# Performance work log

Measured on AMD Instinct MI355X. Metric: run time of the kernel, lower is better.

Reference implementation:

```python
import jax, jax.numpy as jnp
import numpy as np

N, IN, H, OUT, E = 4096, 128, 128, 2, 131072


def _hgnn(x, G, W, b):
    # HGNNConv (Feng et al.): X' = G @ (X W + b), G dense normalized [N,N]
    return G @ (x @ W + b)


def _mha(xin, Wqkv, bqkv, Wo, bo, nh):
    # torch.nn.MultiheadAttention, input (L, B, E), self-attention, eval mode
    L, B, Emb = xin.shape
    hd = Emb // nh
    qkv = xin @ Wqkv.T + bqkv                       # [L,B,3E]
    q, k, v = jnp.split(qkv, 3, axis=-1)
    def sh(t):
        return t.reshape(L, B, nh, hd).transpose(1, 2, 0, 3)  # [B,nh,L,hd]
    q, k, v = sh(q), sh(k), sh(v)
    att = jax.nn.softmax(jnp.einsum('bnld,bnmd->bnlm', q, k) / jnp.sqrt(jnp.float32(hd)), axis=-1)
    o = jnp.einsum('bnlm,bnmd->bnld', att, v).transpose(2, 0, 1, 3).reshape(L, B, Emb)
    return o @ Wo.T + bo


def setup_inputs() -> dict:
    key = jax.random.key(0)
    ks = jax.random.split(key, 40)
    d = {}
    d['x'] = jax.random.normal(ks[0], (N, IN), jnp.float32)
    # dense normalized hypergraph propagation matrices (rand, scaled ~1/N so rows sum ~1)
    d['hg_1hop'] = jax.random.uniform(ks[1], (N, N), jnp.float32) * (2.0 / N)
    d['hg_3hop'] = jax.random.uniform(ks[2], (N, N), jnp.float32) * (2.0 / N)
    d['edge_indices'] = jax.random.randint(ks[3], (2, E), 0, N).astype(jnp.int32)
    d['new_idb'] = jax.random.permutation(ks[4], N).astype(jnp.int32)
    d['lam'] = jax.random.uniform(ks[5], (1,), jnp.float32)
    d['beta'] = jnp.asarray(0.3, jnp.float32)
    i = 6
    def w(shape, s):
        nonlocal i
        out = jax.random.normal(ks[i], shape, jnp.float32) * s
        i += 1
        return out
    sw = 1.0 / np.sqrt(H)
    d['W1'] = w((IN, H), 1.0 / np.sqrt(IN)); d['b1'] = w((H,), 0.01)
    for nm in ['W2', 'W3', 'W1h', 'W3h', 'W2m', 'W3m']:
        d[nm] = w((H, H), sw); d['b' + nm[1:]] = w((H,), 0.01)
    for tag in ['mix', 'fus']:
        d['Wqkv_' + tag] = w((3 * H, H), sw); d['bqkv_' + tag] = w((3 * H,), 0.01)
        d['Wo_' + tag] = w((H, H), sw); d['bo_' + tag] = w((H,), 0.01)
    d['Wc'] = w((2 * H, OUT), 1.0 / np.sqrt(2 * H)); d['bc'] = w((OUT,), 0.01)
    return d


def reference(x, hg_1hop, hg_3hop, edge_indices, new_idb, lam, beta,
              W1, b1, W2, b2, W3, b3, W1h, b1h, W3h, b3h, W2m, b2m, W3m, b3m,
              Wqkv_mix, bqkv_mix, Wo_mix, bo_mix,
              Wqkv_fus, bqkv_fus, Wo_fus, bo_fus, Wc, bc):
    # eval mode: dropout = identity
    h1 = jax.nn.relu(_hgnn(x, hg_1hop, W1, b1))
    h2 = jax.nn.relu(_hgnn(h1, hg_1hop, W2, b2) + h1)
    h3_c1 = jax.nn.relu(_hgnn(h2, hg_1hop, W3, b3) + h2)

    # shuffle_hypergraph: permute nodes of the dense incidence-derived matrix
    hg1_b = hg_1hop[new_idb][:, new_idb]
    hg3_b = hg_3hop[new_idb][:, new_idb]
    l = lam[0]
    # mixup_hidden: manifold mixup of propagated features with permuted graph/features
    h1_mix_1hop = l * _hgnn(h1, hg_1hop, W1h, b1h) + (1.0 - l) * _hgnn(h1[new_idb], hg1_b, W1h, b1h)
    h1_mix_3hop = l * _hgnn(h1, hg_3hop, W3h, b3h) + (1.0 - l) * _hgnn(h1[new_idb], hg3_b, W3h, b3h)

    h1_stack = jnp.stack([h1_mix_1hop, h1_mix_3hop], axis=0)     # [2,N,H]
    h1_mix = _mha(h1_stack, Wqkv_mix, bqkv_mix, Wo_mix, bo_mix, 2).mean(axis=0)
    h2_mix = jax.nn.relu(_hgnn(h1_mix, hg_1hop, W2m, b2m) + h1_mix)
    h3_c2 = jax.nn.relu(_hgnn(h2_mix, hg_1hop, W3m, b3m) + h2_mix) * beta

    h3_stack = jnp.stack([h3_c1, h3_c2], axis=0)                 # [2,N,H]
    h3 = _mha(h3_stack, Wqkv_fus, bqkv_fus, Wo_fus, bo_fus, 4).mean(axis=0)

    edge_emb = jnp.concatenate([h3[edge_indices[0]], h3[edge_indices[1]]], axis=1)  # [E,2H]
    edge_pred = edge_emb @ Wc + bc
    return edge_pred, h3
```

## Files before the change

kernel.cpp:

```cpp
#include <hip/hip_runtime.h>
#include <math.h>

typedef unsigned short u16;
typedef short s8v __attribute__((ext_vector_type(8)));
typedef float f4v __attribute__((ext_vector_type(4)));

__device__ inline float b2f(u16 u) {
    union { unsigned int i; float f; } v; v.i = ((unsigned int)u) << 16; return v.f;
}
__device__ inline u16 f2b(float f) {
    unsigned int x = __float_as_uint(f);
    return (u16)((x + 0x7fffu + ((x >> 16) & 1u)) >> 16);
}
__device__ inline float ldf(const void* p, size_t i, int f32) {
    return f32 ? ((const float*)p)[i] : b2f(((const u16*)p)[i]);
}
__device__ inline s8v load8(const void* p, size_t idx, int f32) {
    if (f32) {
        const float* f = (const float*)p + idx;
        float4 a = *(const float4*)(f);
        float4 b = *(const float4*)(f + 4);
        s8v r;
        r[0] = (short)f2b(a.x); r[1] = (short)f2b(a.y);
        r[2] = (short)f2b(a.z); r[3] = (short)f2b(a.w);
        r[4] = (short)f2b(b.x); r[5] = (short)f2b(b.y);
        r[6] = (short)f2b(b.z); r[7] = (short)f2b(b.w);
        return r;
    }
    return *(const s8v*)((const u16*)p + idx);
}

__global__ void detect_kernel(const u16* __restrict__ hg, int* __restrict__ flag) {
    int lane = threadIdx.x;
    bool ok = true;
    for (int i = 0; i < 32; ++i) {
        float v = b2f(hg[lane * 32 + i]);
        ok = ok && (fabsf(v) <= 1e-3f);
    }
    unsigned long long m = __ballot(ok);
    if (lane == 0) *flag = (m == ~0ull) ? 0 : 1;
}

__global__ __launch_bounds__(512) void big_gemm(const void* __restrict__ G,
                                                const u16* __restrict__ Zt,
                                                float* __restrict__ part,
                                                int kChunkLen,
                                                const int* __restrict__ dflag) {
    __shared__ u16 At[128 * 72];
    __shared__ u16 Bt[128 * 72];
    const int f32 = *dflag;
    const int tid = threadIdx.x;
    const int rowBase = blockIdx.x * 128;
    const int kChunk = blockIdx.y * kChunkLen;
    const int w = tid >> 6, lane = tid & 63;
    const int wm = w & 1, wn = w >> 1;
    const int l15 = lane & 15, quad = lane >> 4;
    const int nIter = kChunkLen >> 6;

    const int r0 = tid >> 3, kb0 = tid & 7;
    const int r1 = 64 + (tid >> 3), kb1 = tid & 7;

    f4v acc[4][2] = {};

    for (int it = 0; it < nIter; ++it) {
        const int kBase = kChunk + it * 64;
        s8v ga0 = load8(G, (size_t)(rowBase + r0) * 4096 + kBase + kb0 * 8, f32);
        s8v gb0 = *(const s8v*)(Zt + (size_t)r0 * 4096 + kBase + kb0 * 8);
        s8v ga1 = load8(G, (size_t)(rowBase + r1) * 4096 + kBase + kb1 * 8, f32);
        s8v gb1 = *(const s8v*)(Zt + (size_t)r1 * 4096 + kBase + kb1 * 8);
        __syncthreads();
        *(s8v*)(At + r0 * 72 + kb0 * 8) = ga0;
        *(s8v*)(Bt + r0 * 72 + kb0 * 8) = gb0;
        *(s8v*)(At + r1 * 72 + kb1 * 8) = ga1;
        *(s8v*)(Bt + r1 * 72 + kb1 * 8) = gb1;
        __syncthreads();
#pragma unroll
        for (int ks = 0; ks < 2; ++ks) {
            s8v a[4], b[2];
            const int kq = ks * 4 + quad;
#pragma unroll
            for (int mi = 0; mi < 4; ++mi)
                a[mi] = *(const s8v*)(At + (wm * 64 + mi * 16 + l15) * 72 + kq * 8);
#pragma unroll
            for (int ni = 0; ni < 2; ++ni)
                b[ni] = *(const s8v*)(Bt + (wn * 32 + ni * 16 + l15) * 72 + kq * 8);
#pragma unroll
            for (int mi = 0; mi < 4; ++mi)
#pragma unroll
                for (int ni = 0; ni < 2; ++ni)
                    acc[mi][ni] = __builtin_amdgcn_mfma_f32_16x16x32_bf16(
                        a[mi], b[ni], acc[mi][ni], 0, 0, 0);
        }
    }
    float* pbase = part + (size_t)blockIdx.y * 4096 * 128;
#pragma unroll
    for (int mi = 0; mi < 4; ++mi)
#pragma unroll
        for (int ni = 0; ni < 2; ++ni) {
            int row = rowBase + wm * 64 + mi * 16 + quad * 4;
            int col = wn * 32 + ni * 16 + l15;
#pragma unroll
            for (int r = 0; r < 4; ++r)
                pbase[(size_t)(row + r) * 128 + col] = acc[mi][ni][r];
        }
}

__global__ __launch_bounds__(256) void reduce_epi(const float* __restrict__ part,
                                                  const u16* __restrict__ res,
                                                  const void* __restrict__ betap,
                                                  u16* __restrict__ out, int mode,
                                                  int S, const int* __restrict__ dflag) {
    int i = (blockIdx.x * 256 + threadIdx.x) * 4;
    f4v t = {};
    for (int s = 0; s < S; ++s)
        t += *(const f4v*)(part + (size_t)s * 524288 + i);
    float bscale = (mode == 2) ? ldf(betap, 0, *dflag) : 1.0f;
    u16 o[4];
#pragma unroll
    for (int j = 0; j < 4; ++j) {
        float v = t[j];
        if (mode == 1 || mode == 2) v += b2f(res[i + j]);
        if (mode <= 2) v = fmaxf(v, 0.0f);
        if (mode == 2) v *= bscale;
        o[j] = f2b(v);
    }
    *(ushort4*)(out + i) = make_ushort4(o[0], o[1], o[2], o[3]);
}

__global__ __launch_bounds__(256) void feat_gemm(const void* __restrict__ A,
                                                 const void* __restrict__ W,
                                                 const void* __restrict__ bias,
                                                 void* __restrict__ out,
                                                 u16* __restrict__ mirror,
                                                 size_t outOfs,
                                                 int M, int NcTotal, int wLayout,
                                                 int outMode, int aRaw, int outRaw,
                                                 const int* __restrict__ dflag) {
    __shared__ char smem[52224];
    u16* Wt = (u16*)smem;
    u16* At = (u16*)(smem + 34816);
    u16* Tt = (u16*)smem;
    const int f32 = *dflag;
    const int aF32 = aRaw & f32;
    const int tid = threadIdx.x;
    const int rowBase = blockIdx.x * 64;
    const int colBase = blockIdx.y * 128;

    if (wLayout == 1) {
#pragma unroll
        for (int i = 0; i < 8; ++i) {
            int c = i * 256 + tid;
            int n = c >> 4, kb = c & 15;
            s8v v = load8(W, (size_t)(colBase + n) * 128 + kb * 8, f32);
            *(s8v*)(Wt + n * 136 + kb * 8) = v;
        }
    } else {
#pragma unroll
        for (int i = 0; i < 64; ++i) {
            int idx = i * 256 + tid;
            int k = idx >> 7, n = idx & 127;
            Wt[n * 136 + k] = f2b(ldf(W, (size_t)k * NcTotal + colBase + n, f32));
        }
    }
#pragma unroll
    for (int i = 0; i < 4; ++i) {
        int c = i * 256 + tid;
        int r = c >> 4, kb = c & 15;
        s8v v = load8(A, (size_t)(rowBase + r) * 128 + kb * 8, aF32);
        *(s8v*)(At + r * 136 + kb * 8) = v;
    }
    __syncthreads();

    const int w = tid >> 6, lane = tid & 63, l15 = lane & 15, quad = lane >> 4;
    f4v acc[8] = {};
#pragma unroll
    for (int ks = 0; ks < 4; ++ks) {
        int k = ks * 32 + quad * 8;
        s8v a = *(const s8v*)(At + (w * 16 + l15) * 136 + k);
#pragma unroll
        for (int ni = 0; ni < 8; ++ni) {
            s8v b = *(const s8v*)(Wt + (ni * 16 + l15) * 136 + k);
            acc[ni] = __builtin_amdgcn_mfma_f32_16x16x32_bf16(a, b, acc[ni], 0, 0, 0);
        }
    }

    if (outMode == 0) {
#pragma unroll
        for (int ni = 0; ni < 8; ++ni) {
            int n = colBase + ni * 16 + l15;
            float bv = ldf(bias, n, f32);
#pragma unroll
            for (int r = 0; r < 4; ++r) {
                int row = rowBase + w * 16 + quad * 4 + r;
                size_t idx = (size_t)row * NcTotal + n;
                float v = acc[ni][r] + bv;
                u16 vb = f2b(v);
                if (outRaw && f32) ((float*)out)[outOfs + idx] = v;
                else               ((u16*)out)[outOfs + idx] = vb;
                if (mirror) mirror[idx] = vb;
            }
        }
    } else {
        __syncthreads();
#pragma unroll
        for (int ni = 0; ni < 8; ++ni) {
            int n = ni * 16 + l15;
            float bv = ldf(bias, colBase + n, f32);
#pragma unroll
            for (int r = 0; r < 4; ++r)
                Tt[n * 72 + (w * 16 + quad * 4 + r)] = f2b(acc[ni][r] + bv);
        }
        __syncthreads();
#pragma unroll
        for (int i = 0; i < 4; ++i) {
            int c = i * 256 + tid;
            int h = c >> 3, nb = c & 7;
            s8v v = *(const s8v*)(Tt + h * 72 + nb * 8);
            *(s8v*)((u16*)out + (size_t)(colBase + h) * M + rowBase + nb * 8) = v;
        }
    }
}

__global__ __launch_bounds__(256) void mix_kernel(const u16* __restrict__ Ph1,
                                                  const u16* __restrict__ Ph3,
                                                  const int* __restrict__ perm,
                                                  const void* __restrict__ lamp,
                                                  u16* __restrict__ xin,
                                                  const int* __restrict__ dflag) {
    int i = blockIdx.x * 256 + threadIdx.x;
    int n = i >> 7, h = i & 127;
    float l = ldf(lamp, 0, *dflag);
    int pn = perm[n];
    float a = l * b2f(Ph1[i]) + (1.0f - l) * b2f(Ph1[(size_t)pn * 128 + h]);
    float b = l * b2f(Ph3[i]) + (1.0f - l) * b2f(Ph3[(size_t)pn * 128 + h]);
    xin[i] = f2b(a);
    xin[524288 + i] = f2b(b);
}

__global__ __launch_bounds__(256) void attn_kernel(const u16* __restrict__ qkv,
                                                   u16* __restrict__ obar, int nh) {
    int wid = threadIdx.x >> 6, lane = threadIdx.x & 63;
    int n = blockIdx.x * 4 + wid;
    const u16* r0 = qkv + (size_t)n * 384;
    const u16* r1 = qkv + (size_t)(4096 + n) * 384;
    int hd = 128 / nh;
    float scale = 1.0f / sqrtf((float)hd);
    float ov[2];
#pragma unroll
    for (int e = 0; e < 2; ++e) {
        int h = e * 64 + lane;
        float q0 = b2f(r0[h]),       q1 = b2f(r1[h]);
        float k0 = b2f(r0[128 + h]), k1 = b2f(r1[128 + h]);
        float v0 = b2f(r0[256 + h]), v1 = b2f(r1[256 + h]);
        float s00 = q0 * k0, s01 = q0 * k1, s10 = q1 * k0, s11 = q1 * k1;
        for (int off = hd >> 1; off; off >>= 1) {
            s00 += __shfl_xor(s00, off);
            s01 += __shfl_xor(s01, off);
            s10 += __shfl_xor(s10, off);
            s11 += __shfl_xor(s11, off);
        }
        s00 *= scale; s01 *= scale; s10 *= scale; s11 *= scale;
        float m0 = fmaxf(s00, s01), m1 = fmaxf(s10, s11);
        float e00 = expf(s00 - m0), e01 = expf(s01 - m0);
        float e10 = expf(s10 - m1), e11 = expf(s11 - m1);
        float a00 = e00 / (e00 + e01), a01 = e01 / (e00 + e01);
        float a10 = e10 / (e10 + e11), a11 = e11 / (e10 + e11);
        float o0 = a00 * v0 + a01 * v1;
        float o1 = a10 * v0 + a11 * v1;
        ov[e] = 0.5f * (o0 + o1);
    }
    obar[(size_t)n * 128 + lane] = f2b(ov[0]);
    obar[(size_t)n * 128 + 64 + lane] = f2b(ov[1]);
}

__global__ __launch_bounds__(256) void edge_kernel(const u16* __restrict__ h3,
                                                   const int* __restrict__ eidx,
                                                   const void* __restrict__ Wc,
                                                   const void* __restrict__ bc,
                                                   void* __restrict__ out,
                                                   const int* __restrict__ dflag) {
    __shared__ float w0[256], w1[256];
    const int f32 = *dflag;
    int t = threadIdx.x;
    w0[t] = ldf(Wc, (size_t)t * 2, f32);
    w1[t] = ldf(Wc, (size_t)t * 2 + 1, f32);
    __syncthreads();
    int e = blockIdx.x * 256 + t;
    float a0 = ldf(bc, 0, f32), a1 = ldf(bc, 1, f32);
#pragma unroll
    for (int p = 0; p < 2; ++p) {
        int node = eidx[p * 131072 + e];
        const s8v* row = (const s8v*)(h3 + (size_t)node * 128);
#pragma unroll
        for (int cch = 0; cch < 16; ++cch) {
            s8v d = row[cch];
#pragma unroll
            for (int j = 0; j < 8; ++j) {
                float f = b2f((u16)d[j]);
                int k = p * 128 + cch * 8 + j;
                a0 += f * w0[k];
                a1 += f * w1[k];
            }
        }
    }
    if (f32) {
        ((float*)out)[(size_t)e * 2] = a0;
        ((float*)out)[(size_t)e * 2 + 1] = a1;
    } else {
        ((u16*)out)[(size_t)e * 2] = f2b(a0);
        ((u16*)out)[(size_t)e * 2 + 1] = f2b(a1);
    }
}

extern "C" void kernel_launch(void* const* d_in, const int* in_sizes, int n_in,
                              void* d_out, int out_size, void* d_ws, size_t ws_size,
                              hipStream_t stream) {
    const void* x    = d_in[0];
    const void* G1   = d_in[1];
    const void* G3   = d_in[2];
    const int* eidx = (const int*)d_in[3];
    const int* perm = (const int*)d_in[4];
    const void* lam  = d_in[5];
    const void* beta = d_in[6];
    const void* W1 = d_in[7],  *b1 = d_in[8];
    const void* W2 = d_in[9],  *b2 = d_in[10];
    const void* W3 = d_in[11], *b3 = d_in[12];
    const void* W1h = d_in[13], *b1h = d_in[14];
    const void* W3h = d_in[15], *b3h = d_in[16];
    const void* W2m = d_in[17], *b2m = d_in[18];
    const void* W3m = d_in[19], *b3m = d_in[20];
    const void* Wqkv_mix = d_in[21], *bqkv_mix = d_in[22];
    const void* Wo_mix   = d_in[23], *bo_mix   = d_in[24];
    const void* Wqkv_fus = d_in[25], *bqkv_fus = d_in[26];
    const void* Wo_fus   = d_in[27], *bo_fus   = d_in[28];
    const void* Wc = d_in[29], *bc = d_in[30];

    const size_t MB = 1ull << 20;
    char* base = (char*)d_ws;
    u16* Zt    = (u16*)(base + 0 * MB);
    u16* h1    = (u16*)(base + 1 * MB);
    u16* h2    = (u16*)(base + 2 * MB);
    u16* h3c1  = (u16*)(base + 3 * MB);
    u16* h1mix = (u16*)(base + 4 * MB);
    u16* h2mix = (u16*)(base + 5 * MB);
    u16* h3c2  = (u16*)(base + 6 * MB);
    u16* Ph1   = (u16*)(base + 7 * MB);
    u16* Ph3   = (u16*)(base + 8 * MB);
    int* dflag = (int*)(base + 9 * MB);
    char* pool = base + 9 * MB + 65536;
    size_t poolBytes = (ws_size > 9 * MB + 65536) ? ws_size - 9 * MB - 65536 : 0;
    int S = (poolBytes >= 16 * MB) ? 8 : (poolBytes >= 8 * MB) ? 4
          : (poolBytes >= 4 * MB) ? 2 : 1;
    int kLen = 4096 / S;
    float* part = (float*)pool;
    u16* xin  = (u16*)pool;
    u16* qkv  = (u16*)(pool + 2 * MB);
    u16* obar = (u16*)pool;

    auto feat = [&](const void* A, const void* W, const void* b, void* o,
                    u16* mir, size_t ofs, int M, int Nc, int wl, int om,
                    int aRaw, int oRaw) {
        feat_gemm<<<dim3(M / 64, Nc / 128), 256, 0, stream>>>(
            A, W, b, o, mir, ofs, M, Nc, wl, om, aRaw, oRaw, dflag);
    };
    auto big = [&](const void* Gm) {
        big_gemm<<<dim3(32, S), 512, 0, stream>>>(Gm, Zt, part, kLen, dflag);
    };
    auto epi = [&](const u16* res, u16* o, int mode) {
        reduce_epi<<<512, 256, 0, stream>>>(part, res, beta, o, mode, S, dflag);
    };

    detect_kernel<<<1, 64, 0, stream>>>((const u16*)G1, dflag);

    feat(x, W1, b1, Zt, nullptr, 0, 4096, 128, 0, 1, 1, 0);  big(G1);  epi(nullptr, h1, 0);
    feat(h1, W2, b2, Zt, nullptr, 0, 4096, 128, 0, 1, 0, 0); big(G1);  epi(h1, h2, 1);
    feat(h1, W1h, b1h, Zt, nullptr, 0, 4096, 128, 0, 1, 0, 0); big(G1); epi(nullptr, Ph1, 3);
    feat(h1, W3h, b3h, Zt, nullptr, 0, 4096, 128, 0, 1, 0, 0); big(G3); epi(nullptr, Ph3, 3);
    feat(h2, W3, b3, Zt, nullptr, 0, 4096, 128, 0, 1, 0, 0); big(G1);  epi(h2, h3c1, 1);
    mix_kernel<<<2048, 256, 0, stream>>>(Ph1, Ph3, perm, lam, xin, dflag);
    feat(xin, Wqkv_mix, bqkv_mix, qkv, nullptr, 0, 8192, 384, 1, 0, 0, 0);
    attn_kernel<<<1024, 256, 0, stream>>>(qkv, obar, 2);
    feat(obar, Wo_mix, bo_mix, h1mix, nullptr, 0, 4096, 128, 1, 0, 0, 0);
    feat(h1mix, W2m, b2m, Zt, nullptr, 0, 4096, 128, 0, 1, 0, 0); big(G1); epi(h1mix, h2mix, 1);
    feat(h2mix, W3m, b3m, Zt, nullptr, 0, 4096, 128, 0, 1, 0, 0); big(G1); epi(h2mix, h3c2, 2);
    feat(h3c1, Wqkv_fus, bqkv_fus, qkv, nullptr, 0, 4096, 384, 1, 0, 0, 0);
    feat(h3c2, Wqkv_fus, bqkv_fus, qkv + (size_t)4096 * 384, nullptr, 0, 4096, 384, 1, 0, 0, 0);
    attn_kernel<<<1024, 256, 0, stream>>>(qkv, obar, 4);
    feat(obar, Wo_fus, bo_fus, d_out, Zt, (size_t)131072 * 2, 4096, 128, 1, 0, 0, 1);
    edge_kernel<<<512, 256, 0, stream>>>(Zt, eidx, Wc, bc, d_out, dflag);
}
```

Before: 643.4 us.

## Batch independent HGNN GEMMs, preconvert G1 to bf16, prefetch, fuse mixup into QKV

The host schedule is rebuilt. The three independent propagations that take h1 now run as one batched feat/big/epi launch via blockIdx.z, so fewer launches and more parallel blocks are needed. When the workspace is large enough, G1 is converted once to a bf16 copy, which avoids reconverting fp32 on each of the six G1 GEMMs. The big GEMM switches to a 64-row tile with register prefetch of the next k-slice and changes its split-K factor. The mixup kernel is folded into the QKV feature GEMM's A-load. The added costs are extra workspace, a conversion pass over G1, and more split-K partial traffic.

```diff
diff --git a/kernel.cpp b/kernel.cpp
--- a/kernel.cpp
+++ b/kernel.cpp
@@ -30,144 +30,193 @@
     return *(const s8v*)((const u16*)p + idx);
 }
 
-__global__ void detect_kernel(const u16* __restrict__ hg, int* __restrict__ flag) {
-    int lane = threadIdx.x;
-    bool ok = true;
-    for (int i = 0; i < 32; ++i) {
-        float v = b2f(hg[lane * 32 + i]);
-        ok = ok && (fabsf(v) <= 1e-3f);
-    }
-    unsigned long long m = __ballot(ok);
-    if (lane == 0) *flag = (m == ~0ull) ? 0 : 1;
-}
-
-__global__ __launch_bounds__(512) void big_gemm(const void* __restrict__ G,
-                                                const u16* __restrict__ Zt,
-                                                float* __restrict__ part,
-                                                int kChunkLen,
-                                                const int* __restrict__ dflag) {
-    __shared__ u16 At[128 * 72];
+__global__ __launch_bounds__(256) void convert_g1(const void* __restrict__ G1,
+                                                  u16* __restrict__ G1b,
+                                                  int* __restrict__ dflag,
+                                                  int doCopy) {
+    __shared__ int s_flag;
+    const int tid = threadIdx.x, bid = blockIdx.x;
+    if (tid == 0) s_flag = 0;
+    __syncthreads();
+    {
+        int bad = 0;
+        for (int i = tid; i < 2048; i += 256) {
+            float v = b2f(((const u16*)G1)[i]);
+            if (!(fabsf(v) <= 1e-3f)) bad = 1;
+        }
+        if (bad) atomicOr(&s_flag, 1);
+    }
+    __syncthreads();
+    const int f32 = s_flag;
+    if (bid == 0 && tid == 0) *dflag = f32;
+    if (!doCopy) return;
+    const int gid = bid * 256 + tid;
+    for (size_t c = (size_t)gid; c < 2097152; c += 262144)
+        *(s8v*)(G1b + c * 8) = load8(G1, c * 8, f32);
+}
+
+struct BigJob { const void* G; const u16* Zt; float* part; int gF32; };
+struct BigP { BigJob j[3]; };
+
+__global__ __launch_bounds__(256) void big_v2(BigP P, int kLen,
+                                              const int* __restrict__ dflag) {
+    __shared__ u16 At[64 * 72];
     __shared__ u16 Bt[128 * 72];
-    const int f32 = *dflag;
+    const BigJob jb = P.j[blockIdx.z];
+    const int f32 = jb.gF32 ? *dflag : 0;
     const int tid = threadIdx.x;
-    const int rowBase = blockIdx.x * 128;
-    const int kChunk = blockIdx.y * kChunkLen;
+    const int rowBase = blockIdx.x * 64;
+    const int kChunk = blockIdx.y * kLen;
+    const int nIter = kLen >> 6;
     const int w = tid >> 6, lane = tid & 63;
     const int wm = w & 1, wn = w >> 1;
     const int l15 = lane & 15, quad = lane >> 4;
-    const int nIter = kChunkLen >> 6;
-
-    const int r0 = tid >> 3, kb0 = tid & 7;
-    const int r1 = 64 + (tid >> 3), kb1 = tid & 7;
-
-    f4v acc[4][2] = {};
-
+    const int rA0 = tid >> 3, rA1 = 32 + (tid >> 3), kb = tid & 7;
+    const u16* Zt = jb.Zt;
+
+    f4v acc[2][4] = {};
+    s8v a0, a1, b0, b1, b2, b3;
+    {
+        const int kBase = kChunk;
+        a0 = load8(jb.G, (size_t)(rowBase + rA0) * 4096 + kBase + kb * 8, f32);
+        a1 = load8(jb.G, (size_t)(rowBase + rA1) * 4096 + kBase + kb * 8, f32);
+        b0 = *(const s8v*)(Zt + (size_t)(rA0) * 4096 + kBase + kb * 8);
+        b1 = *(const s8v*)(Zt + (size_t)(rA0 + 32) * 4096 + kBase + kb * 8);
+        b2 = *(const s8v*)(Zt + (size_t)(rA0 + 64) * 4096 + kBase + kb * 8);
+        b3 = *(const s8v*)(Zt + (size_t)(rA0 + 96) * 4096 + kBase + kb * 8);
+    }
     for (int it = 0; it < nIter; ++it) {
-        const int kBase = kChunk + it * 64;
-        s8v ga0 = load8(G, (size_t)(rowBase + r0) * 4096 + kBase + kb0 * 8, f32);
-        s8v gb0 = *(const s8v*)(Zt + (size_t)r0 * 4096 + kBase + kb0 * 8);
-        s8v ga1 = load8(G, (size_t)(rowBase + r1) * 4096 + kBase + kb1 * 8, f32);
-        s8v gb1 = *(const s8v*)(Zt + (size_t)r1 * 4096 + kBase + kb1 * 8);
         __syncthreads();
-        *(s8v*)(At + r0 * 72 + kb0 * 8) = ga0;
-        *(s8v*)(Bt + r0 * 72 + kb0 * 8) = gb0;
-        *(s8v*)(At + r1 * 72 + kb1 * 8) = ga1;
-        *(s8v*)(Bt + r1 * 72 + kb1 * 8) = gb1;
+        *(s8v*)(At + rA0 * 72 + kb * 8) = a0;
+        *(s8v*)(At + rA1 * 72 + kb * 8) = a1;
+        *(s8v*)(Bt + rA0 * 72 + kb * 8) = b0;
+        *(s8v*)(Bt + (rA0 + 32) * 72 + kb * 8) = b1;
+        *(s8v*)(Bt + (rA0 + 64) * 72 + kb * 8) = b2;
+        *(s8v*)(Bt + (rA0 + 96) * 72 + kb * 8) = b3;
         __syncthreads();
+        if (it + 1 < nIter) {
+            const int kBase = kChunk + (it + 1) * 64;
+            a0 = load8(jb.G, (size_t)(rowBase + rA0) * 4096 + kBase + kb * 8, f32);
+            a1 = load8(jb.G, (size_t)(rowBase + rA1) * 4096 + kBase + kb * 8, f32);
+            b0 = *(const s8v*)(Zt + (size_t)(rA0) * 4096 + kBase + kb * 8);
+            b1 = *(const s8v*)(Zt + (size_t)(rA0 + 32) * 4096 + kBase + kb * 8);
+            b2 = *(const s8v*)(Zt + (size_t)(rA0 + 64) * 4096 + kBase + kb * 8);
+            b3 = *(const s8v*)(Zt + (size_t)(rA0 + 96) * 4096 + kBase + kb * 8);
+        }
 #pragma unroll
         for (int ks = 0; ks < 2; ++ks) {
-            s8v a[4], b[2];
-            const int kq = ks * 4 + quad;
-#pragma unroll
-            for (int mi = 0; mi < 4; ++mi)
-                a[mi] = *(const s8v*)(At + (wm * 64 + mi * 16 + l15) * 72 + kq * 8);
-#pragma unroll
-            for (int ni = 0; ni < 2; ++ni)
-                b[ni] = *(const s8v*)(Bt + (wn * 32 + ni * 16 + l15) * 72 + kq * 8);
-#pragma unroll
-            for (int mi = 0; mi < 4; ++mi)
-#pragma unroll
-                for (int ni = 0; ni < 2; ++ni)
+            s8v af[2], bf[4];
+            const int ko = (ks * 4 + quad) * 8;
+#pragma unroll
+            for (int mi = 0; mi < 2; ++mi)
+                af[mi] = *(const s8v*)(At + (wm * 32 + mi * 16 + l15) * 72 + ko);
+#pragma unroll
+            for (int ni = 0; ni < 4; ++ni)
+                bf[ni] = *(const s8v*)(Bt + (wn * 64 + ni * 16 + l15) * 72 + ko);
+#pragma unroll
+            for (int mi = 0; mi < 2; ++mi)
+#pragma unroll
+                for (int ni = 0; ni < 4; ++ni)
                     acc[mi][ni] = __builtin_amdgcn_mfma_f32_16x16x32_bf16(
-                        a[mi], b[ni], acc[mi][ni], 0, 0, 0);
-        }
-    }
-    float* pbase = part + (size_t)blockIdx.y * 4096 * 128;
-#pragma unroll
-    for (int mi = 0; mi < 4; ++mi)
-#pragma unroll
-        for (int ni = 0; ni < 2; ++ni) {
-            int row = rowBase + wm * 64 + mi * 16 + quad * 4;
-            int col = wn * 32 + ni * 16 + l15;
+                        af[mi], bf[ni], acc[mi][ni], 0, 0, 0);
+        }
+    }
+    float* pbase = jb.part + (size_t)blockIdx.y * 524288;
+#pragma unroll
+    for (int mi = 0; mi < 2; ++mi)
+#pragma unroll
+        for (int ni = 0; ni < 4; ++ni) {
+            int row = rowBase + wm * 32 + mi * 16 + quad * 4;
+            int col = wn * 64 + ni * 16 + l15;
 #pragma unroll
             for (int r = 0; r < 4; ++r)
                 pbase[(size_t)(row + r) * 128 + col] = acc[mi][ni][r];
         }
 }
 
-__global__ __launch_bounds__(256) void reduce_epi(const float* __restrict__ part,
-                                                  const u16* __restrict__ res,
-                                                  const void* __restrict__ betap,
-                                                  u16* __restrict__ out, int mode,
-                                                  int S, const int* __restrict__ dflag) {
+struct EpiJob { const float* part; const u16* res; u16* out; int mode; };
+struct EpiP { EpiJob j[3]; const void* betap; };
+
+__global__ __launch_bounds__(256) void epi_v2(EpiP P, int S,
+                                              const int* __restrict__ dflag) {
+    const EpiJob J = P.j[blockIdx.z];
     int i = (blockIdx.x * 256 + threadIdx.x) * 4;
     f4v t = {};
     for (int s = 0; s < S; ++s)
-        t += *(const f4v*)(part + (size_t)s * 524288 + i);
-    float bscale = (mode == 2) ? ldf(betap, 0, *dflag) : 1.0f;
+        t += *(const f4v*)(J.part + (size_t)s * 524288 + i);
+    float bscale = (J.mode == 2) ? ldf(P.betap, 0, *dflag) : 1.0f;
     u16 o[4];
 #pragma unroll
-    for (int j = 0; j < 4; ++j) {
-        float v = t[j];
-        if (mode == 1 || mode == 2) v += b2f(res[i + j]);
-        if (mode <= 2) v = fmaxf(v, 0.0f);
-        if (mode == 2) v *= bscale;
-        o[j] = f2b(v);
-    }
-    *(ushort4*)(out + i) = make_ushort4(o[0], o[1], o[2], o[3]);
-}
-
-__global__ __launch_bounds__(256) void feat_gemm(const void* __restrict__ A,
-                                                 const void* __restrict__ W,
-                                                 const void* __restrict__ bias,
-                                                 void* __restrict__ out,
-                                                 u16* __restrict__ mirror,
-                                                 size_t outOfs,
-                                                 int M, int NcTotal, int wLayout,
-                                                 int outMode, int aRaw, int outRaw,
-                                                 const int* __restrict__ dflag) {
-    __shared__ char smem[52224];
-    u16* Wt = (u16*)smem;
-    u16* At = (u16*)(smem + 34816);
-    u16* Tt = (u16*)smem;
+    for (int k = 0; k < 4; ++k) {
+        float v = t[k];
+        if (J.mode == 1 || J.mode == 2) v += b2f(J.res[i + k]);
+        if (J.mode <= 2) v = fmaxf(v, 0.0f);
+        if (J.mode == 2) v *= bscale;
+        o[k] = f2b(v);
+    }
+    *(ushort4*)(J.out + i) = make_ushort4(o[0], o[1], o[2], o[3]);
+}
+
+struct FeatJob { const void* A; const void* W; const void* bias; void* out;
+                 u16* mir; size_t outOfs; int wLayout; int outMode; int aMode; };
+struct FeatP { FeatJob j[3]; const u16* Ph1; const u16* Ph3;
+               const int* perm; const void* lam; };
+
+__global__ __launch_bounds__(256) void feat_v2(FeatP P, int M, int NcTotal,
+                                               const int* __restrict__ dflag) {
+    __shared__ char smemf[52224];
+    u16* Wt = (u16*)smemf;
+    u16* At = (u16*)(smemf + 34816);
+    u16* Tt = (u16*)smemf;
+    const FeatJob J = P.j[blockIdx.z];
     const int f32 = *dflag;
-    const int aF32 = aRaw & f32;
     const int tid = threadIdx.x;
     const int rowBase = blockIdx.x * 64;
     const int colBase = blockIdx.y * 128;
 
-    if (wLayout == 1) {
+    if (J.wLayout == 1) {
 #pragma unroll
         for (int i = 0; i < 8; ++i) {
             int c = i * 256 + tid;
             int n = c >> 4, kb = c & 15;
-            s8v v = load8(W, (size_t)(colBase + n) * 128 + kb * 8, f32);
-            *(s8v*)(Wt + n * 136 + kb * 8) = v;
+            *(s8v*)(Wt + n * 136 + kb * 8) =
+                load8(J.W, (size_t)(colBase + n) * 128 + kb * 8, f32);
         }
     } else {
 #pragma unroll
         for (int i = 0; i < 64; ++i) {
             int idx = i * 256 + tid;
             int k = idx >> 7, n = idx & 127;
-            Wt[n * 136 + k] = f2b(ldf(W, (size_t)k * NcTotal + colBase + n, f32));
-        }
-    }
-#pragma unroll
-    for (int i = 0; i < 4; ++i) {
-        int c = i * 256 + tid;
-        int r = c >> 4, kb = c & 15;
-        s8v v = load8(A, (size_t)(rowBase + r) * 128 + kb * 8, aF32);
-        *(s8v*)(At + r * 136 + kb * 8) = v;
+            Wt[n * 136 + k] = f2b(ldf(J.W, (size_t)k * NcTotal + colBase + n, f32));
+        }
+    }
+    if (J.aMode == 2) {
+        float l = ldf(P.lam, 0, f32);
+#pragma unroll
+        for (int i = 0; i < 4; ++i) {
+            int c = i * 256 + tid;
+            int r = c >> 4, kb = c & 15;
+            int grow = rowBase + r;
+            const u16* src = (grow < 4096) ? P.Ph1 : P.Ph3;
+            int n = grow & 4095;
+            int pn = P.perm[n];
+            s8v va = *(const s8v*)(src + (size_t)n * 128 + kb * 8);
+            s8v vb = *(const s8v*)(src + (size_t)pn * 128 + kb * 8);
+            s8v r8;
+#pragma unroll
+            for (int q = 0; q < 8; ++q)
+                r8[q] = (short)f2b(l * b2f((u16)va[q]) + (1.0f - l) * b2f((u16)vb[q]));
+            *(s8v*)(At + r * 136 + kb * 8) = r8;
+        }
+    } else {
+        const int aF32 = (J.aMode == 1) ? f32 : 0;
+#pragma unroll
+        for (int i = 0; i < 4; ++i) {
+            int c = i * 256 + tid;
+            int r = c >> 4, kb = c & 15;
+            *(s8v*)(At + r * 136 + kb * 8) =
+                load8(J.A, (size_t)(rowBase + r) * 128 + kb * 8, aF32);
+        }
     }
     __syncthreads();
 
@@ -184,20 +233,31 @@
         }
     }
 
-    if (outMode == 0) {
+    if (J.outMode == 0) {
 #pragma unroll
         for (int ni = 0; ni < 8; ++ni) {
             int n = colBase + ni * 16 + l15;
-            float bv = ldf(bias, n, f32);
+            float bv = ldf(J.bias, n, f32);
+#pragma unroll
+            for (int r = 0; r < 4; ++r) {
+                int row = rowBase + w * 16 + quad * 4 + r;
+                ((u16*)J.out)[(size_t)row * NcTotal + n] = f2b(acc[ni][r] + bv);
+            }
+        }
+    } else if (J.outMode == 2) {
+#pragma unroll
+        for (int ni = 0; ni < 8; ++ni) {
+            int n = colBase + ni * 16 + l15;
+            float bv = ldf(J.bias, n, f32);
 #pragma unroll
             for (int r = 0; r < 4; ++r) {
                 int row = rowBase + w * 16 + quad * 4 + r;
                 size_t idx = (size_t)row * NcTotal + n;
                 float v = acc[ni][r] + bv;
                 u16 vb = f2b(v);
-                if (outRaw && f32) ((float*)out)[outOfs + idx] = v;
-                else               ((u16*)out)[outOfs + idx] = vb;
-                if (mirror) mirror[idx] = vb;
+                J.mir[idx] = vb;
+                if (f32) ((float*)J.out)[J.outOfs + idx] = v;
+                else     ((u16*)J.out)[J.outOfs + idx] = vb;
             }
         }
     } else {
@@ -205,7 +265,7 @@
 #pragma unroll
         for (int ni = 0; ni < 8; ++ni) {
             int n = ni * 16 + l15;
-            float bv = ldf(bias, colBase + n, f32);
+            float bv = ldf(J.bias, colBase + n, f32);
 #pragma unroll
             for (int r = 0; r < 4; ++r)
                 Tt[n * 72 + (w * 16 + quad * 4 + r)] = f2b(acc[ni][r] + bv);
@@ -216,25 +276,9 @@
             int c = i * 256 + tid;
             int h = c >> 3, nb = c & 7;
             s8v v = *(const s8v*)(Tt + h * 72 + nb * 8);
-            *(s8v*)((u16*)out + (size_t)(colBase + h) * M + rowBase + nb * 8) = v;
-        }
-    }
-}
-
-__global__ __launch_bounds__(256) void mix_kernel(const u16* __restrict__ Ph1,
-                                                  const u16* __restrict__ Ph3,
-                                                  const int* __restrict__ perm,
-                                                  const void* __restrict__ lamp,
-                                                  u16* __restrict__ xin,
-                                                  const int* __restrict__ dflag) {
-    int i = blockIdx.x * 256 + threadIdx.x;
-    int n = i >> 7, h = i & 127;
-    float l = ldf(lamp, 0, *dflag);
-    int pn = perm[n];
-    float a = l * b2f(Ph1[i]) + (1.0f - l) * b2f(Ph1[(size_t)pn * 128 + h]);
-    float b = l * b2f(Ph3[i]) + (1.0f - l) * b2f(Ph3[(size_t)pn * 128 + h]);
-    xin[i] = f2b(a);
-    xin[524288 + i] = f2b(b);
+            *(s8v*)((u16*)J.out + (size_t)(colBase + h) * M + rowBase + nb * 8) = v;
+        }
+    }
 }
 
 __global__ __launch_bounds__(256) void attn_kernel(const u16* __restrict__ qkv,
@@ -265,9 +309,7 @@
         float e10 = expf(s10 - m1), e11 = expf(s11 - m1);
         float a00 = e00 / (e00 + e01), a01 = e01 / (e00 + e01);
         float a10 = e10 / (e10 + e11), a11 = e11 / (e10 + e11);
-        float o0 = a00 * v0 + a01 * v1;
-        float o1 = a10 * v0 + a11 * v1;
-        ov[e] = 0.5f * (o0 + o1);
+        ov[e] = 0.5f * ((a00 * v0 + a01 * v1) + (a10 * v0 + a11 * v1));
     }
     obar[(size_t)n * 128 + lane] = f2b(ov[0]);
     obar[(size_t)n * 128 + 64 + lane] = f2b(ov[1]);
@@ -337,55 +379,105 @@
 
     const size_t MB = 1ull << 20;
     char* base = (char*)d_ws;
-    u16* Zt    = (u16*)(base + 0 * MB);
-    u16* h1    = (u16*)(base + 1 * MB);
-    u16* h2    = (u16*)(base + 2 * MB);
-    u16* h3c1  = (u16*)(base + 3 * MB);
-    u16* h1mix = (u16*)(base + 4 * MB);
-    u16* h2mix = (u16*)(base + 5 * MB);
-    u16* h3c2  = (u16*)(base + 6 * MB);
-    u16* Ph1   = (u16*)(base + 7 * MB);
-    u16* Ph3   = (u16*)(base + 8 * MB);
-    int* dflag = (int*)(base + 9 * MB);
-    char* pool = base + 9 * MB + 65536;
-    size_t poolBytes = (ws_size > 9 * MB + 65536) ? ws_size - 9 * MB - 65536 : 0;
-    int S = (poolBytes >= 16 * MB) ? 8 : (poolBytes >= 8 * MB) ? 4
-          : (poolBytes >= 4 * MB) ? 2 : 1;
-    int kLen = 4096 / S;
-    float* part = (float*)pool;
-    u16* xin  = (u16*)pool;
-    u16* qkv  = (u16*)(pool + 2 * MB);
-    u16* obar = (u16*)pool;
-
-    auto feat = [&](const void* A, const void* W, const void* b, void* o,
-                    u16* mir, size_t ofs, int M, int Nc, int wl, int om,
-                    int aRaw, int oRaw) {
-        feat_gemm<<<dim3(M / 64, Nc / 128), 256, 0, stream>>>(
-            A, W, b, o, mir, ofs, M, Nc, wl, om, aRaw, oRaw, dflag);
+    const bool tier1 = ws_size >= 100 * MB;
+    const int Ssing = tier1 ? 16 : 4;
+    const int Sbat  = tier1 ? 8 : 2;
+    u16* G1b = (u16*)base;
+    char* pool = base + (tier1 ? 32 : 0) * MB;
+    const size_t poolSz = (size_t)(tier1 ? 48 : 12) * MB;
+    char* persist = pool + poolSz;
+    u16* Zt0   = (u16*)(persist + 0 * MB);
+    u16* Zt1   = (u16*)(persist + 1 * MB);
+    u16* Zt2   = (u16*)(persist + 2 * MB);
+    u16* Zt3   = (u16*)(persist + 3 * MB);
+    u16* h1    = (u16*)(persist + 4 * MB);
+    u16* h2    = (u16*)(persist + 5 * MB);
+    u16* h3c1  = (u16*)(persist + 6 * MB);
+    u16* h1mix = (u16*)(persist + 7 * MB);
+    u16* h2mix = (u16*)(persist + 8 * MB);
+    u16* h3c2  = (u16*)(persist + 9 * MB);
+    u16* Ph1   = (u16*)(persist + 10 * MB);
+    u16* Ph3   = (u16*)(persist + 11 * MB);
+    u16* mir   = (u16*)(persist + 12 * MB);
+    u16* qkv   = (u16*)(persist + 13 * MB);
+    int* dflag = (int*)(persist + 19 * MB);
+    float* part0 = (float*)pool;
+    float* part1 = (float*)(pool + (size_t)Sbat * 2 * MB);
+    float* part2 = (float*)(pool + (size_t)2 * Sbat * 2 * MB);
+
+    const void* G1use = tier1 ? (const void*)G1b : G1;
+    const int g1F32 = tier1 ? 0 : 1;
+
+    auto featN = [&](FeatP& FP, int nz, int M, int Nc) {
+        feat_v2<<<dim3(M / 64, Nc / 128, nz), 256, 0, stream>>>(FP, M, Nc, dflag);
     };
-    auto big = [&](const void* Gm) {
-        big_gemm<<<dim3(32, S), 512, 0, stream>>>(Gm, Zt, part, kLen, dflag);
+    auto feat1 = [&](const void* A, const void* W, const void* b, void* o,
+                     int M, int Nc, int wl, int om, int am,
+                     u16* mr = nullptr, size_t ofs = 0) {
+        FeatP FP = {};
+        FP.j[0] = { A, W, b, o, mr, ofs, wl, om, am };
+        FP.Ph1 = Ph1; FP.Ph3 = Ph3; FP.perm = perm; FP.lam = lam;
+        featN(FP, 1, M, Nc);
     };
-    auto epi = [&](const u16* res, u16* o, int mode) {
-        reduce_epi<<<512, 256, 0, stream>>>(part, res, beta, o, mode, S, dflag);
+    auto big1 = [&](const void* Gm, int gF32, const u16* Zt, float* part) {
+        BigP BP = {};
+        BP.j[0] = { Gm, Zt, part, gF32 };
+        big_v2<<<dim3(64, Ssing, 1), 256, 0, stream>>>(BP, 4096 / Ssing, dflag);
     };
-
-    detect_kernel<<<1, 64, 0, stream>>>((const u16*)G1, dflag);
-
-    feat(x, W1, b1, Zt, nullptr, 0, 4096, 128, 0, 1, 1, 0);  big(G1);  epi(nullptr, h1, 0);
-    feat(h1, W2, b2, Zt, nullptr, 0, 4096, 128, 0, 1, 0, 0); big(G1);  epi(h1, h2, 1);
-    feat(h1, W1h, b1h, Zt, nullptr, 0, 4096, 128, 0, 1, 0, 0); big(G1); epi(nullptr, Ph1, 3);
-    feat(h1, W3h, b3h, Zt, nullptr, 0, 4096, 128, 0, 1, 0, 0); big(G3); epi(nullptr, Ph3, 3);
-    feat(h2, W3, b3, Zt, nullptr, 0, 4096, 128, 0, 1, 0, 0); big(G1);  epi(h2, h3c1, 1);
-    mix_kernel<<<2048, 256, 0, stream>>>(Ph1, Ph3, perm, lam, xin, dflag);
-    feat(xin, Wqkv_mix, bqkv_mix, qkv, nullptr, 0, 8192, 384, 1, 0, 0, 0);
-    attn_kernel<<<1024, 256, 0, stream>>>(qkv, obar, 2);
-    feat(obar, Wo_mix, bo_mix, h1mix, nullptr, 0, 4096, 128, 1, 0, 0, 0);
-    feat(h1mix, W2m, b2m, Zt, nullptr, 0, 4096, 128, 0, 1, 0, 0); big(G1); epi(h1mix, h2mix, 1);
-    feat(h2mix, W3m, b3m, Zt, nullptr, 0, 4096, 128, 0, 1, 0, 0); big(G1); epi(h2mix, h3c2, 2);
-    feat(h3c1, Wqkv_fus, bqkv_fus, qkv, nullptr, 0, 4096, 384, 1, 0, 0, 0);
-    feat(h3c2, Wqkv_fus, bqkv_fus, qkv + (size_t)4096 * 384, nullptr, 0, 4096, 384, 1, 0, 0, 0);
-    attn_kernel<<<1024, 256, 0, stream>>>(qkv, obar, 4);
-    feat(obar, Wo_fus, bo_fus, d_out, Zt, (size_t)131072 * 2, 4096, 128, 1, 0, 0, 1);
-    edge_kernel<<<512, 256, 0, stream>>>(Zt, eidx, Wc, bc, d_out, dflag);
-}
+    auto epi1 = [&](const float* part, const u16* res, u16* o, int mode) {
+        EpiP EP = {};
+        EP.j[0] = { part, res, o, mode };
+        EP.betap = beta;
+        epi_v2<<<dim3(512, 1, 1), 256, 0, stream>>>(EP, Ssing, dflag);
+    };
+
+    convert_g1<<<1024, 256, 0, stream>>>(G1, G1b, dflag, tier1 ? 1 : 0);
+    feat1(x, W1, b1, Zt0, 4096, 128, 0, 1, 1);
+    big1(G1use, g1F32, Zt0, part0);
+    epi1(part0, nullptr, h1, 0);
+    {
+        FeatP FP = {};
+        FP.j[0] = { h1, W2,  b2,  Zt1, nullptr, 0, 0, 1, 0 };
+        FP.j[1] = { h1, W1h, b1h, Zt2, nullptr, 0, 0, 1, 0 };
+        FP.j[2] = { h1, W3h, b3h, Zt3, nullptr, 0, 0, 1, 0 };
+        FP.Ph1 = Ph1; FP.Ph3 = Ph3; FP.perm = perm; FP.lam = lam;
+        featN(FP, 3, 4096, 128);
+    }
+    {
+        BigP BP = {};
+        BP.j[0] = { G1use, Zt1, part0, g1F32 };
+        BP.j[1] = { G1use, Zt2, part1, g1F32 };
+        BP.j[2] = { G3,    Zt3, part2, 1 };
+        big_v2<<<dim3(64, Sbat, 3), 256, 0, stream>>>(BP, 4096 / Sbat, dflag);
+    }
+    {
+        EpiP EP = {};
+        EP.j[0] = { part0, h1, h2, 1 };
+        EP.j[1] = { part1, nullptr, Ph1, 3 };
+        EP.j[2] = { part2, nullptr, Ph3, 3 };
+        EP.betap = beta;
+        epi_v2<<<dim3(512, 1, 3), 256, 0, stream>>>(EP, Sbat, dflag);
+    }
+    feat1(h2, W3, b3, Zt0, 4096, 128, 0, 1, 0);
+    big1(G1use, g1F32, Zt0, part0);
+    feat1(nullptr, Wqkv_mix, bqkv_mix, qkv, 8192, 384, 1, 0, 2);
+    epi1(part0, h2, h3c1, 1);
+    attn_kernel<<<1024, 256, 0, stream>>>(qkv, (u16*)Zt0, 2);
+    feat1(Zt0, Wo_mix, bo_mix, h1mix, 4096, 128, 1, 0, 0);
+    feat1(h1mix, W2m, b2m, Zt1, 4096, 128, 0, 1, 0);
+    big1(G1use, g1F32, Zt1, part0);
+    epi1(part0, h1mix, h2mix, 1);
+    feat1(h2mix, W3m, b3m, Zt1, 4096, 128, 0, 1, 0);
+    big1(G1use, g1F32, Zt1, part0);
+    epi1(part0, h2mix, h3c2, 2);
+    {
+        FeatP FP = {};
+        FP.j[0] = { h3c1, Wqkv_fus, bqkv_fus, qkv, nullptr, 0, 1, 0, 0 };
+        FP.j[1] = { h3c2, Wqkv_fus, bqkv_fus, qkv + (size_t)4096 * 384, nullptr, 0, 1, 0, 0 };
+        FP.Ph1 = Ph1; FP.Ph3 = Ph3; FP.perm = perm; FP.lam = lam;
+        featN(FP, 2, 4096, 384);
+    }
+    attn_kernel<<<1024, 256, 0, stream>>>(qkv, (u16*)Zt0, 4);
+    feat1(Zt0, Wo_fus, bo_fus, d_out, 4096, 128, 1, 2, 0, mir, (size_t)131072 * 2);
+    edge_kernel<<<512, 256, 0, stream>>>(mir, eidx, Wc, bc, d_out, dflag);
+}
```

Result: faster. 540.1 us (-16.1%).
